# Performance work log

Hardware: AMD Instinct MI355X
Metric: run time of the kernel (lower is better)

The kernel has to match this reference:

```python
import jax, jax.numpy as jnp
import numpy as np

B, N, C, O, K, D = 32, 2048, 64, 64, 3, 16

def setup_inputs() -> dict:
    key = jax.random.key(0)
    ks = jax.random.split(key, 6)
    x = jax.random.normal(ks[0], (B, N, C), dtype=jnp.float32)
    node_embeddings = jax.random.normal(ks[1], (N, D), dtype=jnp.float32)
    adj_m = jax.random.uniform(ks[2], (N, N), dtype=jnp.float32)
    weights_pool = jax.random.normal(ks[3], (D, K, C, O), dtype=jnp.float32) * 0.1
    bias_pool = jax.random.normal(ks[4], (D, O), dtype=jnp.float32) * 0.1
    sa_weight = jax.random.normal(ks[5], (N, 2 * N), dtype=jnp.float32) * (1.0 / np.sqrt(2 * N))
    return {"x": x, "node_embeddings": node_embeddings, "adj_m": adj_m,
            "weights_pool": weights_pool, "bias_pool": bias_pool, "sa_weight": sa_weight}

def reference(x, node_embeddings, adj_m, weights_pool, bias_pool, sa_weight):
    n = node_embeddings.shape[0]
    # learned adaptive adjacency [N,N]
    supports = jax.nn.softmax(jax.nn.relu(node_embeddings @ node_embeddings.T), axis=1)
    # SpatialAttention: 1x1 conv over 2N channels == matmul with [N,2N] weight
    z = jnp.concatenate([supports, adj_m], axis=1) @ sa_weight.T  # [N,N]
    s2 = jax.nn.sigmoid(z)
    supports = s2 * adj_m + (1.0 - s2) * supports
    # Chebyshev polynomial basis
    support_set = [jnp.eye(n, dtype=supports.dtype), supports]
    for _ in range(2, K):
        support_set.append(2.0 * supports @ support_set[-1] - support_set[-2])
    supports_k = jnp.stack(support_set, axis=0)  # [K,N,N]
    # per-node generated weights/bias from embeddings
    weights = jnp.einsum('nd,dkio->nkio', node_embeddings, weights_pool)  # [N,K,C,O]
    bias = node_embeddings @ bias_pool  # [N,O]
    # graph conv: aggregate then per-node matmul
    x_g = jnp.einsum('knm,bmc->bnkc', supports_k, x)  # [B,N,K,C]
    x_gconv = jnp.einsum('bnki,nkio->bno', x_g, weights) + bias  # [B,N,O]
    return x_gconv
```

## Files before the change

### kernel.cpp

```cpp
#include <hip/hip_runtime.h>


typedef unsigned short u16;
typedef float f32x4 __attribute__((ext_vector_type(4)));
typedef __bf16 bf16x8 __attribute__((ext_vector_type(8)));
typedef unsigned short u16x8 __attribute__((ext_vector_type(8)));

__device__ __forceinline__ u16 f2bf(float f) {
    unsigned u = __float_as_uint(f);
    u += 0x7FFFu + ((u >> 16) & 1u);
    return (u16)(u >> 16);
}
__device__ __forceinline__ float bf2f(u16 h) {
    return __uint_as_float((unsigned)h << 16);
}
__device__ __forceinline__ void gl_lds16(const void* g, void* l) {
    __builtin_amdgcn_global_load_lds(
        (const __attribute__((address_space(1))) unsigned*)g,
        (__attribute__((address_space(3))) unsigned*)l, 16, 0, 0);
}

__global__ __launch_bounds__(256)
void supports_softmax(const float* __restrict__ E, u16* __restrict__ Acat,
                      u16* __restrict__ supC) {
    const int n = blockIdx.x, tid = threadIdx.x;
    const int lane = tid & 63, wave = tid >> 6;
    __shared__ float red[4];
    float e[16];
#pragma unroll
    for (int d = 0; d < 16; ++d) e[d] = E[n * 16 + d];
    float v[8];
    float mx = 0.f;
#pragma unroll
    for (int r = 0; r < 8; ++r) {
        int m = r * 256 + tid;
        const float4* Er = (const float4*)(E + (size_t)m * 16);
        float4 a = Er[0], b = Er[1], c = Er[2], d4 = Er[3];
        float s = 0.f;
        s = fmaf(a.x, e[0], s);  s = fmaf(a.y, e[1], s);
        s = fmaf(a.z, e[2], s);  s = fmaf(a.w, e[3], s);
        s = fmaf(b.x, e[4], s);  s = fmaf(b.y, e[5], s);
        s = fmaf(b.z, e[6], s);  s = fmaf(b.w, e[7], s);
        s = fmaf(c.x, e[8], s);  s = fmaf(c.y, e[9], s);
        s = fmaf(c.z, e[10], s); s = fmaf(c.w, e[11], s);
        s = fmaf(d4.x, e[12], s); s = fmaf(d4.y, e[13], s);
        s = fmaf(d4.z, e[14], s); s = fmaf(d4.w, e[15], s);
        s = fmaxf(s, 0.f);
        v[r] = s;
        mx = fmaxf(mx, s);
    }
    for (int off = 32; off; off >>= 1) mx = fmaxf(mx, __shfl_down(mx, off, 64));
    if (lane == 0) red[wave] = mx;
    __syncthreads();
    mx = fmaxf(fmaxf(red[0], red[1]), fmaxf(red[2], red[3]));
    __syncthreads();
    float sum = 0.f;
#pragma unroll
    for (int r = 0; r < 8; ++r) { v[r] = __expf(v[r] - mx); sum += v[r]; }
    for (int off = 32; off; off >>= 1) sum += __shfl_down(sum, off, 64);
    if (lane == 0) red[wave] = sum;
    __syncthreads();
    sum = red[0] + red[1] + red[2] + red[3];
    float inv = 1.f / sum;
#pragma unroll
    for (int r = 0; r < 8; ++r) {
        u16 o = f2bf(v[r] * inv);
        Acat[(size_t)n * 4096 + r * 256 + tid] = o;
        supC[(size_t)n * 2048 + r * 256 + tid] = o;
    }
}

__global__ __launch_bounds__(256)
void cast_adj(const float* __restrict__ adj, u16* __restrict__ Acat) {
    size_t j = ((size_t)blockIdx.x * 256 + threadIdx.x) * 4;
    float4 v = *(const float4*)(adj + j);
    int n = (int)(j >> 11), c = (int)(j & 2047);
    ushort4 o = make_ushort4(f2bf(v.x), f2bf(v.y), f2bf(v.z), f2bf(v.w));
    *(ushort4*)(Acat + (size_t)n * 4096 + 2048 + c) = o;
}

__global__ __launch_bounds__(256)
void cast_bf16_vec(const float* __restrict__ in, u16* __restrict__ out) {
    size_t j = ((size_t)blockIdx.x * 256 + threadIdx.x) * 4;
    float4 v = *(const float4*)(in + j);
    ushort4 o = make_ushort4(f2bf(v.x), f2bf(v.y), f2bf(v.z), f2bf(v.w));
    *(ushort4*)(out + j) = o;
}

__global__ __launch_bounds__(256)
void transpose_bf16(const u16* __restrict__ in, u16* __restrict__ out) {
    __shared__ u16 t[64][65];
    int bx = blockIdx.x * 64, by = blockIdx.y * 64;
    int c = threadIdx.x & 63, g = threadIdx.x >> 6;
#pragma unroll
    for (int r = 0; r < 16; ++r) {
        int row = g * 16 + r;
        t[row][c] = in[(size_t)(by + row) * 2048 + bx + c];
    }
    __syncthreads();
#pragma unroll
    for (int r = 0; r < 16; ++r) {
        int row = g * 16 + r;
        out[(size_t)(bx + row) * 2048 + by + c] = t[c][row];
    }
}

__global__ __launch_bounds__(256)
void build_xtT(const float* __restrict__ x, u16* __restrict__ xtT) {
    __shared__ u16 t[64][65];
    int b = blockIdx.y, m0 = blockIdx.x * 64;
    int c = threadIdx.x & 63, g = threadIdx.x >> 6;
#pragma unroll
    for (int r = 0; r < 16; ++r) {
        int mm = g * 16 + r;
        t[mm][c] = f2bf(x[((size_t)b * 2048 + m0 + mm) * 64 + c]);
    }
    __syncthreads();
#pragma unroll
    for (int r = 0; r < 16; ++r) {
        int cc = g * 16 + r;
        xtT[((size_t)b * 64 + cc) * 2048 + m0 + c] = t[c][cc];
    }
}

template <int MODE>
__global__ __launch_bounds__(256, 4)
void gemm_bt(const u16* __restrict__ A, const u16* __restrict__ Bt,
             float* __restrict__ Cf, u16* __restrict__ Cb,
             int M, int N, int K, int Kh) {
    __shared__ alignas(16) u16 As[128 * 64];
    __shared__ alignas(16) u16 Bs[64 * 64];
    const int tid = threadIdx.x, lane = tid & 63, wave = tid >> 6;
    const int m0 = blockIdx.y * 128, n0 = blockIdx.x * 64;
    const int wm = (wave >> 1) * 64, wn = (wave & 1) * 32;
    const int kbeg = blockIdx.z * Kh, kend = kbeg + Kh;
    const int ml = lane & 15, c0l = lane >> 4;
    f32x4 acc[4][2] = {};

    int baseA[4], mskA[4], baseB[2], mskB[2];
#pragma unroll
    for (int i = 0; i < 4; ++i) { int m = wm + i * 16 + ml; baseA[i] = m * 8; mskA[i] = m & 7; }
#pragma unroll
    for (int j = 0; j < 2; ++j) { int nn = wn + j * 16 + ml; baseB[j] = nn * 8; mskB[j] = nn & 7; }

    for (int k0 = kbeg; k0 < kend; k0 += 64) {
#pragma unroll
        for (int r = 0; r < 4; ++r) {
            int s = wave * 64 + r * 256 + lane;
            int row = s >> 3, gc = (s & 7) ^ (row & 7);
            u16* lds = As + (wave * 64 + r * 256) * 8;
            gl_lds16(A + (size_t)(m0 + row) * K + k0 + gc * 8, lds);
        }
#pragma unroll
        for (int r = 0; r < 2; ++r) {
            int s = wave * 64 + r * 256 + lane;
            int row = s >> 3, gc = (s & 7) ^ (row & 7);
            u16* lds = Bs + (wave * 64 + r * 256) * 8;
            gl_lds16(Bt + (size_t)(n0 + row) * K + k0 + gc * 8, lds);
        }
        __syncthreads();
#pragma unroll
        for (int ks8 = 0; ks8 < 8; ks8 += 4) {
            bf16x8 af[4], bv[2];
#pragma unroll
            for (int i = 0; i < 4; ++i)
                af[i] = *(const bf16x8*)(As + (baseA[i] + ((c0l + ks8) ^ mskA[i])) * 8);
#pragma unroll
            for (int j = 0; j < 2; ++j)
                bv[j] = *(const bf16x8*)(Bs + (baseB[j] + ((c0l + ks8) ^ mskB[j])) * 8);
#pragma unroll
            for (int i = 0; i < 4; ++i)
#pragma unroll
                for (int j = 0; j < 2; ++j)
                    acc[i][j] = __builtin_amdgcn_mfma_f32_16x16x32_bf16(af[i], bv[j], acc[i][j], 0, 0, 0);
        }
        __syncthreads();
    }

    const int col_l = lane & 15, row_l = (lane >> 4) * 4;
    float* Cfp = Cf + (size_t)blockIdx.z * M * N;
#pragma unroll
    for (int i = 0; i < 4; ++i)
#pragma unroll
        for (int j = 0; j < 2; ++j)
#pragma unroll
            for (int r = 0; r < 4; ++r) {
                int row = m0 + wm + i * 16 + row_l + r;
                int col = n0 + wn + j * 16 + col_l;
                if (MODE == 0) Cfp[(size_t)row * N + col] = acc[i][j][r];
                else           Cb[(size_t)row * N + col] = f2bf(acc[i][j][r]);
            }
}

__global__ __launch_bounds__(256)
void reduce_z(const float* __restrict__ p, const float* __restrict__ adj,
              const u16* __restrict__ supC, u16* __restrict__ S) {
    size_t j = ((size_t)blockIdx.x * 256 + threadIdx.x) * 4;
    float4 a = *(const float4*)(p + j);
    float4 b = *(const float4*)(p + (size_t)2048 * 2048 + j);
    float4 ad = *(const float4*)(adj + j);
    ushort4 sp = *(const ushort4*)(supC + j);
    float z0 = a.x + b.x, z1 = a.y + b.y, z2 = a.z + b.z, z3 = a.w + b.w;
    float s0 = 1.f / (1.f + __expf(-z0)), s1 = 1.f / (1.f + __expf(-z1));
    float s2 = 1.f / (1.f + __expf(-z2)), s3 = 1.f / (1.f + __expf(-z3));
    ushort4 o = make_ushort4(
        f2bf(s0 * ad.x + (1.f - s0) * bf2f(sp.x)),
        f2bf(s1 * ad.y + (1.f - s1) * bf2f(sp.y)),
        f2bf(s2 * ad.z + (1.f - s2) * bf2f(sp.z)),
        f2bf(s3 * ad.w + (1.f - s3) * bf2f(sp.w)));
    *(ushort4*)(S + j) = o;
}

__global__ __launch_bounds__(256)
void reduce_t2(const float* __restrict__ p, u16* __restrict__ T2) {
    size_t j = ((size_t)blockIdx.x * 256 + threadIdx.x) * 4;
    float4 a = *(const float4*)(p + j);
    float4 b = *(const float4*)(p + (size_t)2048 * 2048 + j);
    int row = (int)(j >> 11), col = (int)(j & 2047);
    float v[4] = {2.f * (a.x + b.x), 2.f * (a.y + b.y),
                  2.f * (a.z + b.z), 2.f * (a.w + b.w)};
#pragma unroll
    for (int t = 0; t < 4; ++t) if (row == col + t) v[t] -= 1.f;
    *(ushort4*)(T2 + j) = make_ushort4(f2bf(v[0]), f2bf(v[1]), f2bf(v[2]), f2bf(v[3]));
}

__global__ __launch_bounds__(256)
void wgen(const float* __restrict__ E, const float* __restrict__ Wp,
          u16* __restrict__ Wn) {
    __shared__ float Es[128 * 16];
    const int tid = threadIdx.x;
    const int c0 = blockIdx.x * 512, nb = blockIdx.y * 128;
    const int i4 = (tid & 127) * 4, ng = tid >> 7;
    for (int j = tid; j < 2048; j += 256) Es[j] = E[nb * 16 + j];
    float4 wpv[16];
#pragma unroll
    for (int d = 0; d < 16; ++d)
        wpv[d] = *(const float4*)(Wp + (size_t)d * 12288 + c0 + i4);
    __syncthreads();
    for (int nl = 0; nl < 64; ++nl) {
        int n = ng * 64 + nl;
        float4 s = make_float4(0.f, 0.f, 0.f, 0.f);
#pragma unroll
        for (int d = 0; d < 16; ++d) {
            float e = Es[n * 16 + d];
            s.x = fmaf(e, wpv[d].x, s.x);
            s.y = fmaf(e, wpv[d].y, s.y);
            s.z = fmaf(e, wpv[d].z, s.z);
            s.w = fmaf(e, wpv[d].w, s.w);
        }
        ushort4 o = make_ushort4(f2bf(s.x), f2bf(s.y), f2bf(s.z), f2bf(s.w));
        *(ushort4*)(Wn + (size_t)(nb + n) * 12288 + c0 + i4) = o;
    }
}

__global__ __launch_bounds__(256)
void gconv(const float* __restrict__ x, const float* __restrict__ E,
           const u16* __restrict__ Wn, const float* __restrict__ bp,
           const u16* __restrict__ xg, float* __restrict__ out) {
    const int n = blockIdx.x, tid = threadIdx.x;
    __shared__ alignas(16) float wl[3 * 64 * 64];
    __shared__ alignas(16) float xl[3 * 32 * 68];
    __shared__ float bl[64];
    for (int j = tid * 8; j < 12288; j += 2048) {
        u16x8 w = *(const u16x8*)(Wn + (size_t)n * 12288 + j);
#pragma unroll
        for (int t = 0; t < 8; ++t) wl[j + t] = bf2f(w[t]);
    }
    if (tid < 64) {
        float s = 0.f;
#pragma unroll
        for (int d = 0; d < 16; ++d) s = fmaf(E[n * 16 + d], bp[d * 64 + tid], s);
        bl[tid] = s;
    }
    for (int j4 = tid; j4 < 512; j4 += 256) {
        int j = j4 * 4, b = j >> 6, i = j & 63;
        int lo = b * 68 + i;
        *(float4*)(xl + lo) = *(const float4*)(x + ((size_t)b * 2048 + n) * 64 + i);
        ushort4 g1 = *(const ushort4*)(xg + (size_t)n * 2048 + j);
        ushort4 g2 = *(const ushort4*)(xg + (size_t)(2048 + n) * 2048 + j);
        *(float4*)(xl + 2176 + lo) = make_float4(bf2f(g1.x), bf2f(g1.y), bf2f(g1.z), bf2f(g1.w));
        *(float4*)(xl + 4352 + lo) = make_float4(bf2f(g2.x), bf2f(g2.y), bf2f(g2.z), bf2f(g2.w));
    }
    __syncthreads();
    const int b = tid >> 3, og = tid & 7;
    float acc[8];
#pragma unroll
    for (int t = 0; t < 8; ++t) acc[t] = bl[og * 8 + t];
    for (int k = 0; k < 3; ++k) {
#pragma unroll 4
        for (int i = 0; i < 64; ++i) {
            float xv = xl[k * 2176 + b * 68 + i];
            const float4 w0 = *(const float4*)(wl + (k * 64 + i) * 64 + og * 8);
            const float4 w1 = *(const float4*)(wl + (k * 64 + i) * 64 + og * 8 + 4);
            acc[0] = fmaf(w0.x, xv, acc[0]); acc[1] = fmaf(w0.y, xv, acc[1]);
            acc[2] = fmaf(w0.z, xv, acc[2]); acc[3] = fmaf(w0.w, xv, acc[3]);
            acc[4] = fmaf(w1.x, xv, acc[4]); acc[5] = fmaf(w1.y, xv, acc[5]);
            acc[6] = fmaf(w1.z, xv, acc[6]); acc[7] = fmaf(w1.w, xv, acc[7]);
        }
    }
    float* op = out + ((size_t)b * 2048 + n) * 64 + og * 8;
    *(float4*)op       = make_float4(acc[0], acc[1], acc[2], acc[3]);
    *((float4*)op + 1) = make_float4(acc[4], acc[5], acc[6], acc[7]);
}

extern "C" void kernel_launch(void* const* d_in, const int* in_sizes, int n_in,
                              void* d_out, int out_size, void* d_ws, size_t ws_size,
                              hipStream_t stream) {
    const float* x   = (const float*)d_in[0];
    const float* E   = (const float*)d_in[1];
    const float* adj = (const float*)d_in[2];
    const float* Wp  = (const float*)d_in[3];
    const float* bp  = (const float*)d_in[4];
    const float* saw = (const float*)d_in[5];
    float* out = (float*)d_out;

    char* ws = (char*)d_ws;
    const size_t MB = 1u << 20;
    u16*   Acat  = (u16*)(ws);
    u16*   sawb  = (u16*)(ws + 16 * MB);
    u16*   XtT   = (u16*)(ws + 32 * MB);
    u16*   supC  = (u16*)(ws + 40 * MB);
    float* zpart = (float*)(ws + 48 * MB);
    u16*   S_bf  = (u16*)(ws);
    u16*   T2_bf = (u16*)(ws + 8 * MB);
    u16*   St    = (u16*)(ws + 16 * MB);
    u16*   xg_bf = (u16*)(ws + 56 * MB);
    u16*   Wn    = (u16*)(ws);

    supports_softmax<<<2048, 256, 0, stream>>>(E, Acat, supC);
    cast_adj<<<4096, 256, 0, stream>>>(adj, Acat);
    cast_bf16_vec<<<8192, 256, 0, stream>>>(saw, sawb);
    build_xtT<<<dim3(32, 32), 256, 0, stream>>>(x, XtT);

    gemm_bt<0><<<dim3(32, 16, 2), 256, 0, stream>>>(Acat, sawb, zpart, nullptr,
                                                    2048, 2048, 4096, 2048);
    reduce_z<<<4096, 256, 0, stream>>>(zpart, adj, supC, S_bf);
    transpose_bf16<<<dim3(32, 32), 256, 0, stream>>>(S_bf, St);
    gemm_bt<0><<<dim3(32, 16, 2), 256, 0, stream>>>(S_bf, St, zpart, nullptr,
                                                    2048, 2048, 2048, 1024);
    reduce_t2<<<4096, 256, 0, stream>>>(zpart, T2_bf);
    gemm_bt<3><<<dim3(32, 32, 1), 256, 0, stream>>>(S_bf, XtT, nullptr, xg_bf,
                                                    4096, 2048, 2048, 2048);
    wgen<<<dim3(24, 16), 256, 0, stream>>>(E, Wp, Wn);
    gconv<<<2048, 256, 0, stream>>>(x, E, Wn, bp, xg_bf, out);
}
```

Baseline: 337.0 us.

## Apply Chebyshev recurrence to features instead of forming T2 matrix

Replaces the S@S GEMM that builds the 2048x2048 T2 polynomial with a second S@(S@x) GEMM applied to the aggregated features. The identity term is folded into the per-node weights inside gconv (W0-W2, 2*W2). This drops the transpose of S and the T2 reduction, and merges the two cast kernels. gconv now keeps its weights and features in LDS as bf16 to cut shared-memory use. The trade-off is an extra dependent GEMM pass with a split-K reduce and transpose, plus extra bf16 rounding on the intermediate features and the folded weights.

Measured after the change: 331.0 us. Within noise of the previous version (-1.8%).

```diff
diff --git a/kernel.cpp b/kernel.cpp
--- a/kernel.cpp
+++ b/kernel.cpp
@@ -21,8 +21,7 @@
 }
 
 __global__ __launch_bounds__(256)
-void supports_softmax(const float* __restrict__ E, u16* __restrict__ Acat,
-                      u16* __restrict__ supC) {
+void supports_softmax(const float* __restrict__ E, u16* __restrict__ Acat) {
     const int n = blockIdx.x, tid = threadIdx.x;
     const int lane = tid & 63, wave = tid >> 6;
     __shared__ float red[4];
@@ -63,45 +62,25 @@
     sum = red[0] + red[1] + red[2] + red[3];
     float inv = 1.f / sum;
 #pragma unroll
-    for (int r = 0; r < 8; ++r) {
-        u16 o = f2bf(v[r] * inv);
-        Acat[(size_t)n * 4096 + r * 256 + tid] = o;
-        supC[(size_t)n * 2048 + r * 256 + tid] = o;
-    }
-}
-
-__global__ __launch_bounds__(256)
-void cast_adj(const float* __restrict__ adj, u16* __restrict__ Acat) {
-    size_t j = ((size_t)blockIdx.x * 256 + threadIdx.x) * 4;
-    float4 v = *(const float4*)(adj + j);
-    int n = (int)(j >> 11), c = (int)(j & 2047);
-    ushort4 o = make_ushort4(f2bf(v.x), f2bf(v.y), f2bf(v.z), f2bf(v.w));
-    *(ushort4*)(Acat + (size_t)n * 4096 + 2048 + c) = o;
-}
-
-__global__ __launch_bounds__(256)
-void cast_bf16_vec(const float* __restrict__ in, u16* __restrict__ out) {
-    size_t j = ((size_t)blockIdx.x * 256 + threadIdx.x) * 4;
-    float4 v = *(const float4*)(in + j);
-    ushort4 o = make_ushort4(f2bf(v.x), f2bf(v.y), f2bf(v.z), f2bf(v.w));
-    *(ushort4*)(out + j) = o;
-}
-
-__global__ __launch_bounds__(256)
-void transpose_bf16(const u16* __restrict__ in, u16* __restrict__ out) {
-    __shared__ u16 t[64][65];
-    int bx = blockIdx.x * 64, by = blockIdx.y * 64;
-    int c = threadIdx.x & 63, g = threadIdx.x >> 6;
-#pragma unroll
-    for (int r = 0; r < 16; ++r) {
-        int row = g * 16 + r;
-        t[row][c] = in[(size_t)(by + row) * 2048 + bx + c];
-    }
-    __syncthreads();
-#pragma unroll
-    for (int r = 0; r < 16; ++r) {
-        int row = g * 16 + r;
-        out[(size_t)(bx + row) * 2048 + by + c] = t[c][row];
+    for (int r = 0; r < 8; ++r)
+        Acat[(size_t)n * 4096 + r * 256 + tid] = f2bf(v[r] * inv);
+}
+
+__global__ __launch_bounds__(256)
+void cast_inputs(const float* __restrict__ adj, const float* __restrict__ saw,
+                 u16* __restrict__ Acat, u16* __restrict__ sawb) {
+    int bid = blockIdx.x;
+    if (bid < 4096) {
+        size_t j = ((size_t)bid * 256 + threadIdx.x) * 4;
+        float4 v = *(const float4*)(adj + j);
+        int n = (int)(j >> 11), c = (int)(j & 2047);
+        ushort4 o = make_ushort4(f2bf(v.x), f2bf(v.y), f2bf(v.z), f2bf(v.w));
+        *(ushort4*)(Acat + (size_t)n * 4096 + 2048 + c) = o;
+    } else {
+        size_t j = ((size_t)(bid - 4096) * 256 + threadIdx.x) * 4;
+        float4 v = *(const float4*)(saw + j);
+        ushort4 o = make_ushort4(f2bf(v.x), f2bf(v.y), f2bf(v.z), f2bf(v.w));
+        *(ushort4*)(sawb + j) = o;
     }
 }
 
@@ -123,11 +102,9 @@
     }
 }
 
-template <int MODE>
 __global__ __launch_bounds__(256, 4)
 void gemm_bt(const u16* __restrict__ A, const u16* __restrict__ Bt,
-             float* __restrict__ Cf, u16* __restrict__ Cb,
-             int M, int N, int K, int Kh) {
+             float* __restrict__ Cf, int M, int N, int K, int Kh) {
     __shared__ alignas(16) u16 As[128 * 64];
     __shared__ alignas(16) u16 Bs[64 * 64];
     const int tid = threadIdx.x, lane = tid & 63, wave = tid >> 6;
@@ -187,19 +164,19 @@
             for (int r = 0; r < 4; ++r) {
                 int row = m0 + wm + i * 16 + row_l + r;
                 int col = n0 + wn + j * 16 + col_l;
-                if (MODE == 0) Cfp[(size_t)row * N + col] = acc[i][j][r];
-                else           Cb[(size_t)row * N + col] = f2bf(acc[i][j][r]);
+                Cfp[(size_t)row * N + col] = acc[i][j][r];
             }
 }
 
 __global__ __launch_bounds__(256)
 void reduce_z(const float* __restrict__ p, const float* __restrict__ adj,
-              const u16* __restrict__ supC, u16* __restrict__ S) {
+              const u16* __restrict__ Acat, u16* __restrict__ S) {
     size_t j = ((size_t)blockIdx.x * 256 + threadIdx.x) * 4;
     float4 a = *(const float4*)(p + j);
     float4 b = *(const float4*)(p + (size_t)2048 * 2048 + j);
     float4 ad = *(const float4*)(adj + j);
-    ushort4 sp = *(const ushort4*)(supC + j);
+    int row = (int)(j >> 11), col = (int)(j & 2047);
+    ushort4 sp = *(const ushort4*)(Acat + (size_t)row * 4096 + col);
     float z0 = a.x + b.x, z1 = a.y + b.y, z2 = a.z + b.z, z3 = a.w + b.w;
     float s0 = 1.f / (1.f + __expf(-z0)), s1 = 1.f / (1.f + __expf(-z1));
     float s2 = 1.f / (1.f + __expf(-z2)), s3 = 1.f / (1.f + __expf(-z3));
@@ -212,16 +189,34 @@
 }
 
 __global__ __launch_bounds__(256)
-void reduce_t2(const float* __restrict__ p, u16* __restrict__ T2) {
+void reduceT(const float* __restrict__ p, u16* __restrict__ xg1,
+             u16* __restrict__ xg1T) {
+    __shared__ u16 t[64][65];
+    int bx = blockIdx.x * 64, by = blockIdx.y * 64;
+    int c = threadIdx.x & 63, g = threadIdx.x >> 6;
+#pragma unroll
+    for (int r = 0; r < 16; ++r) {
+        int row = g * 16 + r;
+        size_t idx = (size_t)(by + row) * 2048 + bx + c;
+        u16 v = f2bf(p[idx] + p[(size_t)2048 * 2048 + idx]);
+        xg1[idx] = v;
+        t[row][c] = v;
+    }
+    __syncthreads();
+#pragma unroll
+    for (int r = 0; r < 16; ++r) {
+        int row = g * 16 + r;
+        xg1T[(size_t)(bx + row) * 2048 + by + c] = t[c][row];
+    }
+}
+
+__global__ __launch_bounds__(256)
+void reduce2(const float* __restrict__ p, u16* __restrict__ xg2) {
     size_t j = ((size_t)blockIdx.x * 256 + threadIdx.x) * 4;
     float4 a = *(const float4*)(p + j);
     float4 b = *(const float4*)(p + (size_t)2048 * 2048 + j);
-    int row = (int)(j >> 11), col = (int)(j & 2047);
-    float v[4] = {2.f * (a.x + b.x), 2.f * (a.y + b.y),
-                  2.f * (a.z + b.z), 2.f * (a.w + b.w)};
-#pragma unroll
-    for (int t = 0; t < 4; ++t) if (row == col + t) v[t] -= 1.f;
-    *(ushort4*)(T2 + j) = make_ushort4(f2bf(v[0]), f2bf(v[1]), f2bf(v[2]), f2bf(v[3]));
+    *(ushort4*)(xg2 + j) = make_ushort4(f2bf(a.x + b.x), f2bf(a.y + b.y),
+                                        f2bf(a.z + b.z), f2bf(a.w + b.w));
 }
 
 __global__ __launch_bounds__(256)
@@ -253,49 +248,70 @@
     }
 }
 
-__global__ __launch_bounds__(256)
+__global__ __launch_bounds__(256, 4)
 void gconv(const float* __restrict__ x, const float* __restrict__ E,
            const u16* __restrict__ Wn, const float* __restrict__ bp,
-           const u16* __restrict__ xg, float* __restrict__ out) {
+           const u16* __restrict__ xg1, const u16* __restrict__ xg2,
+           float* __restrict__ out) {
     const int n = blockIdx.x, tid = threadIdx.x;
-    __shared__ alignas(16) float wl[3 * 64 * 64];
-    __shared__ alignas(16) float xl[3 * 32 * 68];
+    __shared__ alignas(16) u16 wl[3 * 64 * 64];
+    __shared__ alignas(16) u16 xl[3 * 32 * 72];
     __shared__ float bl[64];
-    for (int j = tid * 8; j < 12288; j += 2048) {
-        u16x8 w = *(const u16x8*)(Wn + (size_t)n * 12288 + j);
-#pragma unroll
-        for (int t = 0; t < 8; ++t) wl[j + t] = bf2f(w[t]);
-    }
+    const u16* wrow = Wn + (size_t)n * 12288;
+    for (int j = tid * 8; j < 12288; j += 2048)
+        *(u16x8*)(wl + j) = *(const u16x8*)(wrow + j);
     if (tid < 64) {
         float s = 0.f;
 #pragma unroll
         for (int d = 0; d < 16; ++d) s = fmaf(E[n * 16 + d], bp[d * 64 + tid], s);
         bl[tid] = s;
     }
-    for (int j4 = tid; j4 < 512; j4 += 256) {
-        int j = j4 * 4, b = j >> 6, i = j & 63;
-        int lo = b * 68 + i;
-        *(float4*)(xl + lo) = *(const float4*)(x + ((size_t)b * 2048 + n) * 64 + i);
-        ushort4 g1 = *(const ushort4*)(xg + (size_t)n * 2048 + j);
-        ushort4 g2 = *(const ushort4*)(xg + (size_t)(2048 + n) * 2048 + j);
-        *(float4*)(xl + 2176 + lo) = make_float4(bf2f(g1.x), bf2f(g1.y), bf2f(g1.z), bf2f(g1.w));
-        *(float4*)(xl + 4352 + lo) = make_float4(bf2f(g2.x), bf2f(g2.y), bf2f(g2.z), bf2f(g2.w));
+    {
+        const int b = tid >> 3, i = (tid & 7) * 8;
+        *(u16x8*)(xl + 2304 + b * 72 + i) = *(const u16x8*)(xg1 + (size_t)n * 2048 + tid * 8);
+        *(u16x8*)(xl + 4608 + b * 72 + i) = *(const u16x8*)(xg2 + (size_t)n * 2048 + tid * 8);
+        float4 xa = *(const float4*)(x + ((size_t)b * 2048 + n) * 64 + i);
+        float4 xb = *(const float4*)(x + ((size_t)b * 2048 + n) * 64 + i + 4);
+        u16x8 xc;
+        xc[0] = f2bf(xa.x); xc[1] = f2bf(xa.y); xc[2] = f2bf(xa.z); xc[3] = f2bf(xa.w);
+        xc[4] = f2bf(xb.x); xc[5] = f2bf(xb.y); xc[6] = f2bf(xb.z); xc[7] = f2bf(xb.w);
+        *(u16x8*)(xl + b * 72 + i) = xc;
+    }
+    __syncthreads();
+    for (int j = tid * 8; j < 4096; j += 2048) {
+        u16x8 w0 = *(const u16x8*)(wl + j);
+        u16x8 w2 = *(const u16x8*)(wl + 8192 + j);
+        u16x8 o0, o2;
+#pragma unroll
+        for (int t = 0; t < 8; ++t) {
+            float f2 = bf2f(w2[t]);
+            o0[t] = f2bf(bf2f(w0[t]) - f2);
+            o2[t] = f2bf(2.f * f2);
+        }
+        *(u16x8*)(wl + j) = o0;
+        *(u16x8*)(wl + 8192 + j) = o2;
     }
     __syncthreads();
     const int b = tid >> 3, og = tid & 7;
     float acc[8];
 #pragma unroll
     for (int t = 0; t < 8; ++t) acc[t] = bl[og * 8 + t];
+#pragma unroll
     for (int k = 0; k < 3; ++k) {
+        const u16* xr = xl + k * 2304 + b * 72;
+        const u16* wr = wl + k * 4096 + og * 8;
 #pragma unroll 4
         for (int i = 0; i < 64; ++i) {
-            float xv = xl[k * 2176 + b * 68 + i];
-            const float4 w0 = *(const float4*)(wl + (k * 64 + i) * 64 + og * 8);
-            const float4 w1 = *(const float4*)(wl + (k * 64 + i) * 64 + og * 8 + 4);
-            acc[0] = fmaf(w0.x, xv, acc[0]); acc[1] = fmaf(w0.y, xv, acc[1]);
-            acc[2] = fmaf(w0.z, xv, acc[2]); acc[3] = fmaf(w0.w, xv, acc[3]);
-            acc[4] = fmaf(w1.x, xv, acc[4]); acc[5] = fmaf(w1.y, xv, acc[5]);
-            acc[6] = fmaf(w1.z, xv, acc[6]); acc[7] = fmaf(w1.w, xv, acc[7]);
+            float xv = bf2f(xr[i]);
+            u16x8 w = *(const u16x8*)(wr + i * 64);
+            acc[0] = fmaf(bf2f(w[0]), xv, acc[0]);
+            acc[1] = fmaf(bf2f(w[1]), xv, acc[1]);
+            acc[2] = fmaf(bf2f(w[2]), xv, acc[2]);
+            acc[3] = fmaf(bf2f(w[3]), xv, acc[3]);
+            acc[4] = fmaf(bf2f(w[4]), xv, acc[4]);
+            acc[5] = fmaf(bf2f(w[5]), xv, acc[5]);
+            acc[6] = fmaf(bf2f(w[6]), xv, acc[6]);
+            acc[7] = fmaf(bf2f(w[7]), xv, acc[7]);
         }
     }
     float* op = out + ((size_t)b * 2048 + n) * 64 + og * 8;
@@ -319,28 +335,24 @@
     u16*   Acat  = (u16*)(ws);
     u16*   sawb  = (u16*)(ws + 16 * MB);
     u16*   XtT   = (u16*)(ws + 32 * MB);
-    u16*   supC  = (u16*)(ws + 40 * MB);
-    float* zpart = (float*)(ws + 48 * MB);
-    u16*   S_bf  = (u16*)(ws);
-    u16*   T2_bf = (u16*)(ws + 8 * MB);
-    u16*   St    = (u16*)(ws + 16 * MB);
-    u16*   xg_bf = (u16*)(ws + 56 * MB);
-    u16*   Wn    = (u16*)(ws);
-
-    supports_softmax<<<2048, 256, 0, stream>>>(E, Acat, supC);
-    cast_adj<<<4096, 256, 0, stream>>>(adj, Acat);
-    cast_bf16_vec<<<8192, 256, 0, stream>>>(saw, sawb);
+    float* part  = (float*)(ws + 48 * MB);
+    u16*   S_bf  = (u16*)(ws + 16 * MB);
+    u16*   xg1T  = (u16*)(ws + 24 * MB);
+    u16*   xg1_bf= (u16*)(ws);
+    u16*   xg2_bf= (u16*)(ws + 8 * MB);
+    u16*   Wn    = (u16*)(ws + 24 * MB);
+
+    supports_softmax<<<2048, 256, 0, stream>>>(E, Acat);
+    cast_inputs<<<12288, 256, 0, stream>>>(adj, saw, Acat, sawb);
     build_xtT<<<dim3(32, 32), 256, 0, stream>>>(x, XtT);
 
-    gemm_bt<0><<<dim3(32, 16, 2), 256, 0, stream>>>(Acat, sawb, zpart, nullptr,
-                                                    2048, 2048, 4096, 2048);
-    reduce_z<<<4096, 256, 0, stream>>>(zpart, adj, supC, S_bf);
-    transpose_bf16<<<dim3(32, 32), 256, 0, stream>>>(S_bf, St);
-    gemm_bt<0><<<dim3(32, 16, 2), 256, 0, stream>>>(S_bf, St, zpart, nullptr,
-                                                    2048, 2048, 2048, 1024);
-    reduce_t2<<<4096, 256, 0, stream>>>(zpart, T2_bf);
-    gemm_bt<3><<<dim3(32, 32, 1), 256, 0, stream>>>(S_bf, XtT, nullptr, xg_bf,
-                                                    4096, 2048, 2048, 2048);
+    gemm_bt<<<dim3(32, 16, 2), 256, 0, stream>>>(Acat, sawb, part, 2048, 2048, 4096, 2048);
+    reduce_z<<<4096, 256, 0, stream>>>(part, adj, Acat, S_bf);
+    gemm_bt<<<dim3(32, 16, 2), 256, 0, stream>>>(S_bf, XtT, part, 2048, 2048, 2048, 1024);
+    reduceT<<<dim3(32, 32), 256, 0, stream>>>(part, xg1_bf, xg1T);
+    gemm_bt<<<dim3(32, 16, 2), 256, 0, stream>>>(S_bf, xg1T, part, 2048, 2048, 2048, 1024);
+    reduce2<<<4096, 256, 0, stream>>>(part, xg2_bf);
+
     wgen<<<dim3(24, 16), 256, 0, stream>>>(E, Wp, Wn);
-    gconv<<<2048, 256, 0, stream>>>(x, E, Wn, bp, xg_bf, out);
-}
+    gconv<<<2048, 256, 0, stream>>>(x, E, Wn, bp, xg1_bf, xg2_bf, out);
+}
```
